# Kernel optimization log

Hardware: AMD Instinct MI355X
Metric: run time of the kernel (lower is better)

Reference implementation:

```python
import jax, jax.numpy as jnp
import numpy as np
from jax import lax

DIM = 96
D_STATE = 16
D_CONV = 4
EXPAND = 2
D_INNER = EXPAND * DIM           # 192
DT_RANK = (DIM + 15) // 16       # 6
EPS = 1e-5


def _upsample2x_align_corners(x):
    # bilinear, align_corners=True, scale_factor=2 (matches nn.Upsample)
    B, C, H, W = x.shape
    def lin_idx(n_in, n_out):
        pos = jnp.arange(n_out) * ((n_in - 1) / (n_out - 1))
        i0 = jnp.floor(pos).astype(jnp.int32)
        i1 = jnp.minimum(i0 + 1, n_in - 1)
        w = (pos - i0).astype(x.dtype)
        return i0, i1, w
    r0, r1, rw = lin_idx(H, 2 * H)
    c0, c1, cw = lin_idx(W, 2 * W)
    xr = x[:, :, r0, :] * (1 - rw)[None, None, :, None] + x[:, :, r1, :] * rw[None, None, :, None]
    return xr[:, :, :, c0] * (1 - cw) + xr[:, :, :, c1] * cw


def _conv2d(x, w, b, pad):
    y = lax.conv_general_dilated(x, w, (1, 1), [(pad, pad), (pad, pad)],
                                 dimension_numbers=('NCHW', 'OIHW', 'NCHW'))
    return y + b[None, :, None, None]


def _instance_norm(x):
    m = x.mean(axis=(2, 3), keepdims=True)
    v = x.var(axis=(2, 3), keepdims=True)
    return (x - m) * lax.rsqrt(v + EPS)


def _selective_scan(u, dt, A, Bm, Cm, D):
    # u, dt: [B,L,Din]; Bm, Cm: [B,L,N]; A: [Din,N]; D: [Din]
    def step(h, inp):
        u_t, dt_t, B_t, C_t = inp                       # [B,Din],[B,Din],[B,N],[B,N]
        dA = jnp.exp(dt_t[..., None] * A)               # [B,Din,N]
        h = h * dA + (dt_t * u_t)[..., None] * B_t[:, None, :]
        y = jnp.einsum('bdn,bn->bd', h, C_t)
        return h, y
    Bsz, L, Din = u.shape
    h0 = jnp.zeros((Bsz, Din, A.shape[1]), u.dtype)
    xs = (u.swapaxes(0, 1), dt.swapaxes(0, 1), Bm.swapaxes(0, 1), Cm.swapaxes(0, 1))
    _, ys = lax.scan(step, h0, xs)                      # ys: [L,B,Din]
    return ys.swapaxes(0, 1) + u * D


def _mamba(xseq, in_proj_w, conv1d_w, conv1d_b, x_proj_w, dt_proj_w, dt_proj_b,
           A_log, D, out_proj_w):
    # xseq: [B,L,dim]
    xz = xseq @ in_proj_w.T                             # [B,L,2*Din]
    xin, z = jnp.split(xz, 2, axis=-1)
    xc = xin.swapaxes(1, 2)                             # [B,Din,L]
    xc = lax.conv_general_dilated(xc, conv1d_w, (1,), [(D_CONV - 1, 0)],
                                  dimension_numbers=('NCH', 'OIH', 'NCH'),
                                  feature_group_count=D_INNER)
    xc = xc + conv1d_b[None, :, None]
    u = jax.nn.silu(xc.swapaxes(1, 2))                  # [B,L,Din]
    x_dbl = u @ x_proj_w.T                              # [B,L,dt_rank+2N]
    dt, Bm, Cm = jnp.split(x_dbl, [DT_RANK, DT_RANK + D_STATE], axis=-1)
    dt = jax.nn.softplus(dt @ dt_proj_w.T + dt_proj_b)  # [B,L,Din]
    A = -jnp.exp(A_log)                                 # [Din,N]
    y = _selective_scan(u, dt, A, Bm, Cm, D)
    y = y * jax.nn.silu(z)
    return y @ out_proj_w.T                             # [B,L,dim]


def setup_inputs() -> dict:
    key = jax.random.key(0)
    ks = jax.random.split(key, 16)
    s = 0.05
    inp = {
        'x': jax.random.normal(ks[0], (2, DIM, 64, 64), jnp.float32),
        'Hx': jax.random.normal(ks[1], (2, DIM * 2, 128, 128), jnp.float32),
        'conv1_w': jax.random.normal(ks[2], (DIM, DIM * 3, 1, 1), jnp.float32) * s,
        'conv1_b': jax.random.normal(ks[3], (DIM,), jnp.float32) * s,
        'conv2_w': jax.random.normal(ks[4], (DIM, DIM, 3, 3), jnp.float32) * s,
        'conv2_b': jax.random.normal(ks[5], (DIM,), jnp.float32) * s,
        'conv3_w': jax.random.normal(ks[6], (DIM, DIM, 1, 1), jnp.float32) * s,
        'conv3_b': jax.random.normal(ks[7], (DIM,), jnp.float32) * s,
        'in_proj_w': jax.random.normal(ks[8], (2 * D_INNER, DIM), jnp.float32) * s,
        'conv1d_w': jax.random.normal(ks[9], (D_INNER, 1, D_CONV), jnp.float32) * s,
        'conv1d_b': jax.random.normal(ks[10], (D_INNER,), jnp.float32) * s,
        'x_proj_w': jax.random.normal(ks[11], (DT_RANK + 2 * D_STATE, D_INNER), jnp.float32) * s,
        'dt_proj_w': jax.random.normal(ks[12], (D_INNER, DT_RANK), jnp.float32) * s,
        'dt_proj_b': jax.random.normal(ks[13], (D_INNER,), jnp.float32) * 0.1,
        'A_log': jnp.log(jnp.tile(jnp.arange(1, D_STATE + 1, dtype=jnp.float32)[None, :], (D_INNER, 1))),
        'D': jnp.ones((D_INNER,), jnp.float32),
        'out_proj_w': jax.random.normal(ks[14], (DIM, D_INNER), jnp.float32) * s,
    }
    return inp


def reference(x, Hx, conv1_w, conv1_b, conv2_w, conv2_b, conv3_w, conv3_b,
              in_proj_w, conv1d_w, conv1d_b, x_proj_w, dt_proj_w, dt_proj_b,
              A_log, D, out_proj_w):
    up = _upsample2x_align_corners(x)                   # [B,dim,H,W]
    cat = jnp.concatenate([up, Hx], axis=1)             # [B,3*dim,H,W]
    h = _conv2d(cat, conv1_w, conv1_b, 0)
    h = _conv2d(h, conv2_w, conv2_b, 1)
    h = _conv2d(h, conv3_w, conv3_b, 0)
    Lx = jax.nn.selu(_instance_norm(h))                 # [B,dim,H,W]
    B, C, H, W = Lx.shape
    seq = Lx.reshape(B, C, H * W).swapaxes(1, 2)        # [B,L,dim]
    y = _mamba(seq, in_proj_w, conv1d_w, conv1d_b, x_proj_w, dt_proj_w,
               dt_proj_b, A_log, D, out_proj_w)
    return y.swapaxes(1, 2).reshape(B, C, H, W) + Lx
```

## Files before the change

kernel.cpp:

```cpp
#include <hip/hip_runtime.h>
#include <hip/hip_bf16.h>
#include <math.h>

#define LSEQ 16384
#define DIN  192
#define GCH  512
#define TCH  32

typedef float f4v __attribute__((ext_vector_type(4)));
typedef short s8v __attribute__((ext_vector_type(8)));
typedef unsigned short u16x8 __attribute__((ext_vector_type(8)));

__device__ __forceinline__ float siluf(float x) { return x / (1.0f + __expf(-x)); }
__device__ __forceinline__ unsigned short f2bf(float f) {
  unsigned int u = __float_as_uint(f);
  unsigned int r = (u + 0x7FFFu + ((u >> 16) & 1u)) >> 16;
  return (unsigned short)r;
}
__device__ __forceinline__ float bf2f(unsigned short s) {
  return __uint_as_float(((unsigned int)s) << 16);
}

__global__ __launch_bounds__(256) void k_packw(const float* __restrict__ c1w,
    const float* __restrict__ c2w, const float* __restrict__ c3w,
    const float* __restrict__ Win, const float* __restrict__ Wx,
    const float* __restrict__ Wout, unsigned short* __restrict__ P) {
  int i = blockIdx.x * 256 + threadIdx.x;
  if (i >= 184320) return;
  if (i < 27648) { P[i] = f2bf(c1w[i]); return; }
  int j = i - 27648;
  if (j < 82944) {
    int cc = j / 27648, r = j - cc * 27648;
    int kk = r / 3072, r2 = r - kk * 3072;
    int oc = r2 >> 5, icl = r2 & 31;
    int ky = kk / 3, kx = kk - ky * 3;
    P[i] = f2bf(c2w[((oc * 96 + cc * 32 + icl) * 3 + ky) * 3 + kx]);
    return;
  }
  j -= 82944;
  if (j < 9216) { P[i] = f2bf(c3w[j]); return; }
  j -= 9216;
  if (j < 36864) { P[i] = f2bf(Win[j]); return; }
  j -= 36864;
  if (j < 9216) {
    int oc = j / 192, k = j - oc * 192;
    P[i] = (oc < 38) ? f2bf(Wx[oc * 192 + k]) : (unsigned short)0;
    return;
  }
  j -= 9216;
  P[i] = f2bf(Wout[j]);
}

__global__ __launch_bounds__(256) void k_upsample(const float* __restrict__ x, float* __restrict__ up) {
  int idx = blockIdx.x * 256 + threadIdx.x;
  if (idx >= 2 * 96 * LSEQ) return;
  int ow = idx & 127, oh = (idx >> 7) & 127, bc = idx >> 14;
  float pr = oh * (63.0f / 127.0f); int r0 = (int)pr; float rw = pr - (float)r0; int r1 = min(r0 + 1, 63);
  float pc = ow * (63.0f / 127.0f); int c0 = (int)pc; float cw = pc - (float)c0; int c1 = min(c0 + 1, 63);
  const float* xp = x + (size_t)bc * 4096;
  float v00 = xp[r0 * 64 + c0], v01 = xp[r0 * 64 + c1];
  float v10 = xp[r1 * 64 + c0], v11 = xp[r1 * 64 + c1];
  float top = v00 + (v10 - v00) * rw;
  float bot = v01 + (v11 - v01) * rw;
  up[idx] = top + (bot - top) * cw;
}

#define SRC_PLANAR2 0
#define SRC_ROWS    1
#define OUT_BF16R    0
#define OUT_F32P     1
#define OUT_F32R     2
#define OUT_F32P_RES 4
#define OUT_XZ       5

template<int SM, int OM, int NT>
__global__ __launch_bounds__(256) void k_gemm(
    const void* __restrict__ xa, const void* __restrict__ xb, int CA,
    const unsigned short* __restrict__ Wp, const float* __restrict__ bias,
    void* __restrict__ outv, void* __restrict__ outv2, const float* __restrict__ resid,
    int K, int ostride, int ng) {
  __shared__ unsigned short x_t[128 * 96];
  __shared__ unsigned short w_t[NT * 16 * 96];
  Wp += (size_t)blockIdx.y * 96 * K;
  int pxg0 = blockIdx.x * 128;
  int b = pxg0 >> 14, px_in0 = pxg0 & 16383;
  int tid = threadIdx.x, lane = tid & 63, wv = tid >> 6;
  int r = lane & 15, q = lane >> 4;
  f4v acc[2][NT];
#pragma unroll
  for (int mi = 0; mi < 2; mi++)
#pragma unroll
    for (int n = 0; n < NT; n++) acc[mi][n] = (f4v)0.0f;
  int nchunk = K / 96;
  for (int kc = 0; kc < nchunk; kc++) {
    for (int t = tid; t < NT * 16 * 12; t += 256) {
      int row = t / 12, u8 = t - row * 12;
      *(u16x8*)&w_t[row * 96 + u8 * 8] = *(const u16x8*)&Wp[(size_t)row * K + kc * 96 + u8 * 8];
    }
    if (SM == SRC_PLANAR2) {
      const float* A0 = (const float*)xa;
      const float* A1 = (const float*)xb;
      int CB = K - CA;
      for (int t = tid; t < 3072; t += 256) {
        int px4 = t / 96, c_l = t - px4 * 96;
        int c = kc * 96 + c_l;
        const float* sp = (c < CA) ? (A0 + ((size_t)b * CA + c) * LSEQ + px_in0 + px4 * 4)
                                   : (A1 + ((size_t)b * CB + (c - CA)) * LSEQ + px_in0 + px4 * 4);
        float4 v = *(const float4*)sp;
        x_t[(px4 * 4 + 0) * 96 + c_l] = f2bf(v.x);
        x_t[(px4 * 4 + 1) * 96 + c_l] = f2bf(v.y);
        x_t[(px4 * 4 + 2) * 96 + c_l] = f2bf(v.z);
        x_t[(px4 * 4 + 3) * 96 + c_l] = f2bf(v.w);
      }
    } else {
      const unsigned short* X = (const unsigned short*)xa;
      for (int t = tid; t < 1536; t += 256) {
        int rr = t / 12, u8 = t - rr * 12;
        *(u16x8*)&x_t[rr * 96 + u8 * 8] =
            *(const u16x8*)&X[(size_t)(pxg0 + rr) * K + kc * 96 + u8 * 8];
      }
    }
    __syncthreads();
#pragma unroll
    for (int k0 = 0; k0 < 96; k0 += 32) {
      s8v a0 = *(const s8v*)&x_t[((wv * 2 + 0) * 16 + r) * 96 + k0 + q * 8];
      s8v a1 = *(const s8v*)&x_t[((wv * 2 + 1) * 16 + r) * 96 + k0 + q * 8];
#pragma unroll
      for (int n = 0; n < NT; n++) {
        s8v bb = *(const s8v*)&w_t[(n * 16 + r) * 96 + k0 + q * 8];
        acc[0][n] = __builtin_amdgcn_mfma_f32_16x16x32_bf16(a0, bb, acc[0][n], 0, 0, 0);
        acc[1][n] = __builtin_amdgcn_mfma_f32_16x16x32_bf16(a1, bb, acc[1][n], 0, 0, 0);
      }
    }
    __syncthreads();
  }
#pragma unroll
  for (int mi = 0; mi < 2; mi++) {
    int pxl = (wv * 2 + mi) * 16 + q * 4;
    int pxg = pxg0 + pxl;
#pragma unroll
    for (int n = 0; n < NT; n++) {
      int oc = n * 16 + r;
      if (OM == OUT_BF16R) {
        float bv = bias[oc];
        unsigned short* O = (unsigned short*)outv;
#pragma unroll
        for (int g = 0; g < 4; g++)
          O[(size_t)(pxg + g) * 96 + oc] = f2bf(acc[mi][n][g] + bv);
      } else if (OM == OUT_F32P) {
        float bv = bias[oc];
        float* O = (float*)outv;
        float4 o = make_float4(acc[mi][n][0] + bv, acc[mi][n][1] + bv,
                               acc[mi][n][2] + bv, acc[mi][n][3] + bv);
        *(float4*)&O[((size_t)b * 96 + oc) * LSEQ + px_in0 + pxl] = o;
      } else if (OM == OUT_F32P_RES) {
        float* O = (float*)outv;
        size_t ad = ((size_t)b * 96 + oc) * LSEQ + px_in0 + pxl;
        float4 rv = *(const float4*)&resid[ad];
        float4 o = make_float4(acc[mi][n][0] + rv.x, acc[mi][n][1] + rv.y,
                               acc[mi][n][2] + rv.z, acc[mi][n][3] + rv.w);
        *(float4*)&O[ad] = o;
      } else if (OM == OUT_F32R) {
        float* O = (float*)outv;
        int ocg = blockIdx.y * 96 + oc;
        if (ocg < ng) {
#pragma unroll
          for (int g = 0; g < 4; g++)
            O[(size_t)(pxg + g) * ostride + ocg] = acc[mi][n][g];
        }
      } else {
        int ocg = (blockIdx.y & 1) * 96 + oc;
        if (blockIdx.y < 2) {
          float* O = (float*)outv;
#pragma unroll
          for (int g = 0; g < 4; g++)
            O[(size_t)(pxg + g) * 192 + ocg] = acc[mi][n][g];
        } else {
          unsigned short* O = (unsigned short*)outv2;
#pragma unroll
          for (int g = 0; g < 4; g++)
            O[(size_t)(pxg + g) * 192 + ocg] = f2bf(acc[mi][n][g]);
        }
      }
    }
  }
}

__global__ __launch_bounds__(256) void k_conv3x3m(const unsigned short* __restrict__ X,
    const unsigned short* __restrict__ Wp2, const float* __restrict__ bias,
    unsigned short* __restrict__ out) {
  __shared__ unsigned short in_t[3 * 68 * 32];
  __shared__ unsigned short w_t[9 * 96 * 32];
  int bi = blockIdx.x;
  int hx = bi & 1, y = (bi >> 1) & 127, b = bi >> 8;
  int px0 = hx * 64;
  int tid = threadIdx.x, lane = tid & 63, wv = tid >> 6;
  int r = lane & 15, q = lane >> 4;
  f4v acc[6];
#pragma unroll
  for (int n = 0; n < 6; n++) acc[n] = (f4v)0.0f;
  for (int cc = 0; cc < 3; cc++) {
    for (int t = tid; t < 3456; t += 256)
      *(u16x8*)&w_t[t * 8] = *(const u16x8*)&Wp2[cc * 27648 + t * 8];
    for (int t = tid; t < 792; t += 256) {
      int row = t / 264, rem = t - row * 264;
      int c_l = rem >> 2, icq = rem & 3;
      int gy = y - 1 + row, gx = px0 - 1 + c_l;
      u16x8 v = {0, 0, 0, 0, 0, 0, 0, 0};
      if (gy >= 0 && gy < 128 && gx >= 0 && gx < 128)
        v = *(const u16x8*)&X[(((size_t)b * 128 + gy) * 128 + gx) * 96 + cc * 32 + icq * 8];
      *(u16x8*)&in_t[(row * 68 + c_l) * 32 + icq * 8] = v;
    }
    __syncthreads();
#pragma unroll
    for (int kk = 0; kk < 9; kk++) {
      int ky = kk / 3, kx = kk - ky * 3;
      s8v a = *(const s8v*)&in_t[(ky * 68 + wv * 16 + r + kx) * 32 + q * 8];
#pragma unroll
      for (int n = 0; n < 6; n++) {
        s8v bb = *(const s8v*)&w_t[(kk * 96 + n * 16 + r) * 32 + q * 8];
        acc[n] = __builtin_amdgcn_mfma_f32_16x16x32_bf16(a, bb, acc[n], 0, 0, 0);
      }
    }
    __syncthreads();
  }
  size_t rowbase = ((size_t)b * 128 + y) * 128 + px0 + wv * 16 + q * 4;
#pragma unroll
  for (int n = 0; n < 6; n++) {
    int oc = n * 16 + r;
    float bv = bias[oc];
#pragma unroll
    for (int g = 0; g < 4; g++)
      out[(rowbase + g) * 96 + oc] = f2bf(acc[n][g] + bv);
  }
}

__global__ __launch_bounds__(256) void k_stats(const float* __restrict__ h, float* __restrict__ stats) {
  int bc = blockIdx.x;
  const float* p = h + (size_t)bc * LSEQ;
  float s = 0.f, ss = 0.f;
  for (int i = threadIdx.x; i < LSEQ; i += 256) { float v = p[i]; s += v; ss = fmaf(v, v, ss); }
  __shared__ float rs[256], rss[256];
  int tid = threadIdx.x;
  rs[tid] = s; rss[tid] = ss; __syncthreads();
  for (int o = 128; o > 0; o >>= 1) {
    if (tid < o) { rs[tid] += rs[tid + o]; rss[tid] += rss[tid + o]; }
    __syncthreads();
  }
  if (tid == 0) {
    float m = rs[0] * (1.0f / LSEQ);
    float var = rss[0] * (1.0f / LSEQ) - m * m;
    stats[bc * 2] = m;
    stats[bc * 2 + 1] = rsqrtf(fmaxf(var, 0.f) + 1e-5f);
  }
}

__global__ __launch_bounds__(256) void k_normselu2(const float* __restrict__ h,
    const float* __restrict__ stats, float* __restrict__ Lx, unsigned short* __restrict__ LxR) {
  __shared__ float tile[96 * 65];
  int px0 = blockIdx.x * 64, b = blockIdx.y;
  int tid = threadIdx.x;
  const float kS = 1.0507009873554805f, kA = 1.6732632423543772f;
  for (int t = tid; t < 1536; t += 256) {
    int c = t >> 4, p4 = t & 15;
    size_t ga = ((size_t)b * 96 + c) * LSEQ + px0 + p4 * 4;
    float4 v = *(const float4*)&h[ga];
    float m = stats[(b * 96 + c) * 2], rv = stats[(b * 96 + c) * 2 + 1];
    v.x = (v.x - m) * rv; v.y = (v.y - m) * rv; v.z = (v.z - m) * rv; v.w = (v.w - m) * rv;
    v.x = v.x > 0.f ? kS * v.x : kS * kA * expm1f(v.x);
    v.y = v.y > 0.f ? kS * v.y : kS * kA * expm1f(v.y);
    v.z = v.z > 0.f ? kS * v.z : kS * kA * expm1f(v.z);
    v.w = v.w > 0.f ? kS * v.w : kS * kA * expm1f(v.w);
    *(float4*)&Lx[ga] = v;
    tile[c * 65 + p4 * 4 + 0] = v.x;
    tile[c * 65 + p4 * 4 + 1] = v.y;
    tile[c * 65 + p4 * 4 + 2] = v.z;
    tile[c * 65 + p4 * 4 + 3] = v.w;
  }
  __syncthreads();
  for (int t = tid; t < 768; t += 256) {
    int px = t / 12, c8 = t - px * 12;
    u16x8 o;
#pragma unroll
    for (int jj = 0; jj < 8; jj++) o[jj] = f2bf(tile[(c8 * 8 + jj) * 65 + px]);
    *(u16x8*)&LxR[((size_t)b * LSEQ + px0 + px) * 96 + c8 * 8] = o;
  }
}

__global__ __launch_bounds__(256) void k_conv1d(const float* __restrict__ xzx,
    const float* __restrict__ w1d, const float* __restrict__ b1d,
    float* __restrict__ u, unsigned short* __restrict__ uR) {
  int gid = blockIdx.x * 256 + threadIdx.x;
  if (gid >= 2 * LSEQ * DIN) return;
  int d = gid % DIN, bl = gid / DIN;
  int l = bl & (LSEQ - 1);
  float4 w = *(const float4*)&w1d[d * 4];
  float wv[4] = {w.x, w.y, w.z, w.w};
  float acc = b1d[d];
#pragma unroll
  for (int k = 0; k < 4; k++) {
    int lk = l - 3 + k;
    if (lk >= 0) acc = fmaf(wv[k], xzx[(size_t)(bl - 3 + k) * DIN + d], acc);
  }
  float s = siluf(acc);
  u[gid] = s;
  uR[gid] = f2bf(s);
}

__global__ __launch_bounds__(192) void k_scanA(const float* __restrict__ u,
    const float* __restrict__ xdbl, const float* __restrict__ Wdt,
    const float* __restrict__ bdt, const float* __restrict__ Alog,
    float* __restrict__ chA, float* __restrict__ chB) {
  int b = blockIdx.y, g = blockIdx.x, d = threadIdx.x;
  __shared__ float Bs[TCH * 16], Dts[TCH * 8];
  for (int i = d; i < TCH * 16; i += 192) {
    int t = i >> 4, n = i & 15;
    Bs[i] = xdbl[(size_t)(b * LSEQ + g * TCH + t) * 38 + 6 + n];
  }
  for (int i = d; i < TCH * 6; i += 192) {
    int t = i / 6, c = i - t * 6;
    Dts[t * 8 + c] = xdbl[(size_t)(b * LSEQ + g * TCH + t) * 38 + c];
  }
  float ac[16];
#pragma unroll
  for (int n = 0; n < 16; n++) ac[n] = -__expf(Alog[d * 16 + n]);
  float wdt[6];
#pragma unroll
  for (int c = 0; c < 6; c++) wdt[c] = Wdt[d * 6 + c];
  float bd = bdt[d];
  __syncthreads();
  float ap[16], hb[16];
#pragma unroll
  for (int n = 0; n < 16; n++) { ap[n] = 1.f; hb[n] = 0.f; }
  for (int t = 0; t < TCH; t++) {
    size_t base = (size_t)(b * LSEQ + g * TCH + t);
    float uv = u[base * DIN + d];
    float dtraw = bd;
#pragma unroll
    for (int c = 0; c < 6; c++) dtraw = fmaf(Dts[t * 8 + c], wdt[c], dtraw);
    float dtv = dtraw > 20.f ? dtraw : log1pf(__expf(dtraw));
    float du = dtv * uv;
    float bs[16];
    const float4* src = (const float4*)&Bs[t * 16];
#pragma unroll
    for (int qq = 0; qq < 4; qq++) {
      float4 v = src[qq];
      bs[qq * 4] = v.x; bs[qq * 4 + 1] = v.y; bs[qq * 4 + 2] = v.z; bs[qq * 4 + 3] = v.w;
    }
#pragma unroll
    for (int n = 0; n < 16; n++) {
      float e = __expf(dtv * ac[n]);
      ap[n] *= e;
      hb[n] = fmaf(hb[n], e, du * bs[n]);
    }
  }
  size_t co = ((size_t)(b * GCH + g) * DIN + d) * 16;
#pragma unroll
  for (int qq = 0; qq < 4; qq++) {
    ((float4*)(chA + co))[qq] = make_float4(ap[qq * 4], ap[qq * 4 + 1], ap[qq * 4 + 2], ap[qq * 4 + 3]);
    ((float4*)(chB + co))[qq] = make_float4(hb[qq * 4], hb[qq * 4 + 1], hb[qq * 4 + 2], hb[qq * 4 + 3]);
  }
}

__global__ __launch_bounds__(256) void k_scanB(const float* __restrict__ chA,
    const float* __restrict__ chB, float* __restrict__ h0) {
  __shared__ float sa[16 * 17], sb[16 * 17];
  int blk = blockIdx.x;
  int b = blk / DIN, d = blk - b * DIN;
  int tid = threadIdx.x;
  int seg = tid >> 4, n = tid & 15;
  float ca[32], cb[32];
  float aagg = 1.f, bagg = 0.f;
#pragma unroll 8
  for (int j = 0; j < 32; j++) {
    int g = seg * 32 + j;
    size_t off = ((size_t)(b * GCH + g) * DIN + d) * 16 + n;
    float a = chA[off], bb = chB[off];
    ca[j] = a; cb[j] = bb;
    bagg = fmaf(a, bagg, bb);
    aagg *= a;
  }
  sa[n * 17 + seg] = aagg;
  sb[n * 17 + seg] = bagg;
  __syncthreads();
  if (tid < 16) {
    float pa = 1.f, pb = 0.f;
#pragma unroll
    for (int s = 0; s < 16; s++) {
      float ta = sa[tid * 17 + s], tb = sb[tid * 17 + s];
      sa[tid * 17 + s] = pa;
      sb[tid * 17 + s] = pb;
      pb = fmaf(ta, pb, tb);
      pa *= ta;
    }
  }
  __syncthreads();
  float h = sb[n * 17 + seg];
#pragma unroll 8
  for (int j = 0; j < 32; j++) {
    int g = seg * 32 + j;
    size_t off = ((size_t)(b * GCH + g) * DIN + d) * 16 + n;
    h0[off] = h;
    h = fmaf(ca[j], h, cb[j]);
  }
}

__global__ __launch_bounds__(192) void k_scanC(const float* __restrict__ u,
    const float* __restrict__ xdbl, const float* __restrict__ Wdt,
    const float* __restrict__ bdt, const unsigned short* __restrict__ zR,
    const float* __restrict__ Alog, const float* __restrict__ Dp,
    const float* __restrict__ h0, unsigned short* __restrict__ yR) {
  int b = blockIdx.y, g = blockIdx.x, d = threadIdx.x;
  __shared__ float Bs[TCH * 16], Cs[TCH * 16], Dts[TCH * 8];
  for (int i = d; i < TCH * 16; i += 192) {
    int t = i >> 4, n = i & 15;
    size_t rb = (size_t)(b * LSEQ + g * TCH + t) * 38;
    Bs[i] = xdbl[rb + 6 + n];
    Cs[i] = xdbl[rb + 22 + n];
  }
  for (int i = d; i < TCH * 6; i += 192) {
    int t = i / 6, c = i - t * 6;
    Dts[t * 8 + c] = xdbl[(size_t)(b * LSEQ + g * TCH + t) * 38 + c];
  }
  float ac[16];
#pragma unroll
  for (int n = 0; n < 16; n++) ac[n] = -__expf(Alog[d * 16 + n]);
  float wdt[6];
#pragma unroll
  for (int c = 0; c < 6; c++) wdt[c] = Wdt[d * 6 + c];
  float bd = bdt[d];
  float Dd = Dp[d];
  __syncthreads();
  size_t co = ((size_t)(b * GCH + g) * DIN + d) * 16;
  float h[16];
#pragma unroll
  for (int qq = 0; qq < 4; qq++) {
    float4 v = ((const float4*)(h0 + co))[qq];
    h[qq * 4] = v.x; h[qq * 4 + 1] = v.y; h[qq * 4 + 2] = v.z; h[qq * 4 + 3] = v.w;
  }
  for (int t = 0; t < TCH; t++) {
    size_t base = (size_t)(b * LSEQ + g * TCH + t);
    float uv = u[base * DIN + d];
    float zv = bf2f(zR[base * DIN + d]);
    float dtraw = bd;
#pragma unroll
    for (int c = 0; c < 6; c++) dtraw = fmaf(Dts[t * 8 + c], wdt[c], dtraw);
    float dtv = dtraw > 20.f ? dtraw : log1pf(__expf(dtraw));
    float du = dtv * uv;
    float bs[16], cs[16];
    const float4* sb = (const float4*)&Bs[t * 16];
    const float4* sc = (const float4*)&Cs[t * 16];
#pragma unroll
    for (int qq = 0; qq < 4; qq++) {
      float4 vb = sb[qq], vc = sc[qq];
      bs[qq * 4] = vb.x; bs[qq * 4 + 1] = vb.y; bs[qq * 4 + 2] = vb.z; bs[qq * 4 + 3] = vb.w;
      cs[qq * 4] = vc.x; cs[qq * 4 + 1] = vc.y; cs[qq * 4 + 2] = vc.z; cs[qq * 4 + 3] = vc.w;
    }
    float y0 = 0.f, y1 = 0.f, y2 = 0.f, y3 = 0.f;
#pragma unroll
    for (int n = 0; n < 16; n++) {
      float e = __expf(dtv * ac[n]);
      h[n] = fmaf(h[n], e, du * bs[n]);
      float p = h[n] * cs[n];
      if ((n & 3) == 0) y0 += p; else if ((n & 3) == 1) y1 += p;
      else if ((n & 3) == 2) y2 += p; else y3 += p;
    }
    float yv = ((y0 + y1) + (y2 + y3)) + uv * Dd;
    yR[base * DIN + d] = f2bf(yv * siluf(zv));
  }
}

extern "C" void kernel_launch(void* const* d_in, const int* in_sizes, int n_in,
                              void* d_out, int out_size, void* d_ws, size_t ws_size,
                              hipStream_t stream) {
  (void)in_sizes; (void)n_in; (void)out_size; (void)ws_size;
  const float* x    = (const float*)d_in[0];
  const float* Hx   = (const float*)d_in[1];
  const float* c1w  = (const float*)d_in[2];
  const float* c1b  = (const float*)d_in[3];
  const float* c2w  = (const float*)d_in[4];
  const float* c2b  = (const float*)d_in[5];
  const float* c3w  = (const float*)d_in[6];
  const float* c3b  = (const float*)d_in[7];
  const float* Win  = (const float*)d_in[8];
  const float* w1d  = (const float*)d_in[9];
  const float* b1d  = (const float*)d_in[10];
  const float* Wx   = (const float*)d_in[11];
  const float* Wdt  = (const float*)d_in[12];
  const float* bdt  = (const float*)d_in[13];
  const float* Alog = (const float*)d_in[14];
  const float* Dp   = (const float*)d_in[15];
  const float* Wout = (const float*)d_in[16];
  float* out = (float*)d_out;

  float* ws = (float*)d_ws;
  const size_t F = (size_t)2 * 96 * LSEQ;
  const size_t Fh = F / 2;

  float*          b_up = ws;
  float*          b_h3 = ws;
  float*          chA  = ws;
  float*          b_Lx = ws + F;
  unsigned short* R1   = (unsigned short*)(ws + 2 * F);
  unsigned short* R2   = (unsigned short*)(ws + 2 * F + Fh);
  float*          xdbl = ws + 2 * F + Fh;
  float*          xzx  = ws + 3 * F;
  float*          chB  = ws + 3 * F;
  float*          h0b  = ws + 4 * F;
  unsigned short* zRb  = (unsigned short*)(ws + 5 * F);
  unsigned short* R3   = (unsigned short*)(ws + 6 * F);
  float*          b_u  = ws + 7 * F;
  unsigned short* Wp   = (unsigned short*)(ws + 9 * F);
  float*          b_st = ws + 9 * F + 92160;

  k_packw<<<dim3(720), dim3(256), 0, stream>>>(c1w, c2w, c3w, Win, Wx, Wout, Wp);
  k_upsample<<<dim3(12288), dim3(256), 0, stream>>>(x, b_up);
  k_gemm<SRC_PLANAR2, OUT_BF16R, 6><<<dim3(256, 1), dim3(256), 0, stream>>>(
      b_up, Hx, 96, Wp, c1b, R1, nullptr, nullptr, 288, 0, 0);
  k_conv3x3m<<<dim3(512), dim3(256), 0, stream>>>(R1, Wp + 27648, c2b, R2);
  k_gemm<SRC_ROWS, OUT_F32P, 6><<<dim3(256, 1), dim3(256), 0, stream>>>(
      R2, nullptr, 0, Wp + 110592, c3b, b_h3, nullptr, nullptr, 96, 0, 0);
  k_stats<<<dim3(192), dim3(256), 0, stream>>>(b_h3, b_st);
  k_normselu2<<<dim3(256, 2), dim3(256), 0, stream>>>(b_h3, b_st, b_Lx, R1);
  k_gemm<SRC_ROWS, OUT_XZ, 6><<<dim3(256, 4), dim3(256), 0, stream>>>(
      R1, nullptr, 0, Wp + 119808, nullptr, xzx, zRb, nullptr, 96, 192, 0);
  k_conv1d<<<dim3((2 * LSEQ * DIN + 255) / 256), dim3(256), 0, stream>>>(xzx, w1d, b1d, b_u, R3);
  k_gemm<SRC_ROWS, OUT_F32R, 3><<<dim3(256, 1), dim3(256), 0, stream>>>(
      R3, nullptr, 0, Wp + 156672, nullptr, xdbl, nullptr, nullptr, 192, 38, 38);
  k_scanA<<<dim3(GCH, 2), dim3(192), 0, stream>>>(b_u, xdbl, Wdt, bdt, Alog, chA, chB);
  k_scanB<<<dim3(2 * DIN), dim3(256), 0, stream>>>(chA, chB, h0b);
  k_scanC<<<dim3(GCH, 2), dim3(192), 0, stream>>>(b_u, xdbl, Wdt, bdt, zRb, Alog, Dp, h0b, R3);
  k_gemm<SRC_ROWS, OUT_F32P_RES, 6><<<dim3(256, 1), dim3(256), 0, stream>>>(
      R3, nullptr, 0, Wp + 165888, nullptr, out, nullptr, b_Lx, 192, 0, 0);
}
```

Before: 380.6 us.

## Fuse upsample into conv1 GEMM load and streamline scan math

New measurement: 348.7 us. 8.4% less time.

```diff
diff --git a/kernel.cpp b/kernel.cpp
--- a/kernel.cpp
+++ b/kernel.cpp
@@ -11,7 +11,14 @@
 typedef short s8v __attribute__((ext_vector_type(8)));
 typedef unsigned short u16x8 __attribute__((ext_vector_type(8)));
 
-__device__ __forceinline__ float siluf(float x) { return x / (1.0f + __expf(-x)); }
+__device__ __forceinline__ float siluf(float x) { return __fdividef(x, 1.0f + __expf(-x)); }
+__device__ __forceinline__ float fexp2(float x) {
+#if __has_builtin(__builtin_amdgcn_exp2f)
+  return __builtin_amdgcn_exp2f(x);
+#else
+  return __expf(x * 0.69314718056f);
+#endif
+}
 __device__ __forceinline__ unsigned short f2bf(float f) {
   unsigned int u = __float_as_uint(f);
   unsigned int r = (u + 0x7FFFu + ((u >> 16) & 1u)) >> 16;
@@ -51,22 +58,9 @@
   P[i] = f2bf(Wout[j]);
 }
 
-__global__ __launch_bounds__(256) void k_upsample(const float* __restrict__ x, float* __restrict__ up) {
-  int idx = blockIdx.x * 256 + threadIdx.x;
-  if (idx >= 2 * 96 * LSEQ) return;
-  int ow = idx & 127, oh = (idx >> 7) & 127, bc = idx >> 14;
-  float pr = oh * (63.0f / 127.0f); int r0 = (int)pr; float rw = pr - (float)r0; int r1 = min(r0 + 1, 63);
-  float pc = ow * (63.0f / 127.0f); int c0 = (int)pc; float cw = pc - (float)c0; int c1 = min(c0 + 1, 63);
-  const float* xp = x + (size_t)bc * 4096;
-  float v00 = xp[r0 * 64 + c0], v01 = xp[r0 * 64 + c1];
-  float v10 = xp[r1 * 64 + c0], v11 = xp[r1 * 64 + c1];
-  float top = v00 + (v10 - v00) * rw;
-  float bot = v01 + (v11 - v01) * rw;
-  up[idx] = top + (bot - top) * cw;
-}
-
 #define SRC_PLANAR2 0
 #define SRC_ROWS    1
+#define SRC_UPCAT   2
 #define OUT_BF16R    0
 #define OUT_F32P     1
 #define OUT_F32R     2
@@ -111,6 +105,38 @@
         x_t[(px4 * 4 + 1) * 96 + c_l] = f2bf(v.y);
         x_t[(px4 * 4 + 2) * 96 + c_l] = f2bf(v.z);
         x_t[(px4 * 4 + 3) * 96 + c_l] = f2bf(v.w);
+      }
+    } else if (SM == SRC_UPCAT) {
+      const float* X0 = (const float*)xa;
+      const float* HX = (const float*)xb;
+      for (int t = tid; t < 3072; t += 256) {
+        int px4 = t / 96, c_l = t - px4 * 96;
+        int c = kc * 96 + c_l;
+        int pxl = px4 * 4;
+        if (c < 96) {
+          int pxg = px_in0 + pxl;
+          int oh = pxg >> 7, ow0 = pxg & 127;
+          float pr = oh * (63.0f / 127.0f);
+          int r0 = (int)pr; float rw = pr - (float)r0; int r1 = min(r0 + 1, 63);
+          const float* rp0 = X0 + ((size_t)b * 96 + c) * 4096 + r0 * 64;
+          const float* rp1 = X0 + ((size_t)b * 96 + c) * 4096 + r1 * 64;
+#pragma unroll
+          for (int g = 0; g < 4; g++) {
+            int ow = ow0 + g;
+            float pc = ow * (63.0f / 127.0f);
+            int c0 = (int)pc; float cw = pc - (float)c0; int c1 = min(c0 + 1, 63);
+            float v00 = rp0[c0], v01 = rp0[c1], v10 = rp1[c0], v11 = rp1[c1];
+            float top = v00 + (v10 - v00) * rw;
+            float bot = v01 + (v11 - v01) * rw;
+            x_t[(pxl + g) * 96 + c_l] = f2bf(top + (bot - top) * cw);
+          }
+        } else {
+          float4 v = *(const float4*)&HX[((size_t)b * 192 + (c - 96)) * LSEQ + px_in0 + pxl];
+          x_t[(pxl + 0) * 96 + c_l] = f2bf(v.x);
+          x_t[(pxl + 1) * 96 + c_l] = f2bf(v.y);
+          x_t[(pxl + 2) * 96 + c_l] = f2bf(v.z);
+          x_t[(pxl + 3) * 96 + c_l] = f2bf(v.w);
+        }
       }
     } else {
       const unsigned short* X = (const unsigned short*)xa;
@@ -255,22 +281,24 @@
   }
 }
 
+__device__ __forceinline__ float seluf(float v) {
+  const float kS = 1.0507009873554805f, kSA = 1.0507009873554805f * 1.6732632423543772f;
+  return v > 0.f ? kS * v : kSA * (__expf(v) - 1.f);
+}
 __global__ __launch_bounds__(256) void k_normselu2(const float* __restrict__ h,
     const float* __restrict__ stats, float* __restrict__ Lx, unsigned short* __restrict__ LxR) {
   __shared__ float tile[96 * 65];
   int px0 = blockIdx.x * 64, b = blockIdx.y;
   int tid = threadIdx.x;
-  const float kS = 1.0507009873554805f, kA = 1.6732632423543772f;
   for (int t = tid; t < 1536; t += 256) {
     int c = t >> 4, p4 = t & 15;
     size_t ga = ((size_t)b * 96 + c) * LSEQ + px0 + p4 * 4;
     float4 v = *(const float4*)&h[ga];
     float m = stats[(b * 96 + c) * 2], rv = stats[(b * 96 + c) * 2 + 1];
-    v.x = (v.x - m) * rv; v.y = (v.y - m) * rv; v.z = (v.z - m) * rv; v.w = (v.w - m) * rv;
-    v.x = v.x > 0.f ? kS * v.x : kS * kA * expm1f(v.x);
-    v.y = v.y > 0.f ? kS * v.y : kS * kA * expm1f(v.y);
-    v.z = v.z > 0.f ? kS * v.z : kS * kA * expm1f(v.z);
-    v.w = v.w > 0.f ? kS * v.w : kS * kA * expm1f(v.w);
+    v.x = seluf((v.x - m) * rv);
+    v.y = seluf((v.y - m) * rv);
+    v.z = seluf((v.z - m) * rv);
+    v.w = seluf((v.w - m) * rv);
     *(float4*)&Lx[ga] = v;
     tile[c * 65 + p4 * 4 + 0] = v.x;
     tile[c * 65 + p4 * 4 + 1] = v.y;
@@ -307,7 +335,7 @@
   uR[gid] = f2bf(s);
 }
 
-__global__ __launch_bounds__(192) void k_scanA(const float* __restrict__ u,
+__global__ __launch_bounds__(192, 3) void k_scanA(const float* __restrict__ u,
     const float* __restrict__ xdbl, const float* __restrict__ Wdt,
     const float* __restrict__ bdt, const float* __restrict__ Alog,
     float* __restrict__ chA, float* __restrict__ chB) {
@@ -321,25 +349,32 @@
     int t = i / 6, c = i - t * 6;
     Dts[t * 8 + c] = xdbl[(size_t)(b * LSEQ + g * TCH + t) * 38 + c];
   }
-  float ac[16];
-#pragma unroll
-  for (int n = 0; n < 16; n++) ac[n] = -__expf(Alog[d * 16 + n]);
+  float ac2[16];
+#pragma unroll
+  for (int n = 0; n < 16; n++) ac2[n] = -__expf(Alog[d * 16 + n]) * 1.44269504f;
   float wdt[6];
 #pragma unroll
   for (int c = 0; c < 6; c++) wdt[c] = Wdt[d * 6 + c];
   float bd = bdt[d];
+  size_t base0 = (size_t)(b * LSEQ + g * TCH);
+  float uu[TCH];
+#pragma unroll
+  for (int t = 0; t < TCH; t++) uu[t] = u[(base0 + t) * DIN + d];
   __syncthreads();
+  float dtv[TCH];
+#pragma unroll
+  for (int t = 0; t < TCH; t++) {
+    float dr = bd;
+#pragma unroll
+    for (int c = 0; c < 6; c++) dr = fmaf(Dts[t * 8 + c], wdt[c], dr);
+    dtv[t] = dr > 20.f ? dr : __logf(1.f + __expf(dr));
+  }
   float ap[16], hb[16];
 #pragma unroll
   for (int n = 0; n < 16; n++) { ap[n] = 1.f; hb[n] = 0.f; }
   for (int t = 0; t < TCH; t++) {
-    size_t base = (size_t)(b * LSEQ + g * TCH + t);
-    float uv = u[base * DIN + d];
-    float dtraw = bd;
-#pragma unroll
-    for (int c = 0; c < 6; c++) dtraw = fmaf(Dts[t * 8 + c], wdt[c], dtraw);
-    float dtv = dtraw > 20.f ? dtraw : log1pf(__expf(dtraw));
-    float du = dtv * uv;
+    float dl2 = dtv[t] * 1.f;
+    float du = dtv[t] * uu[t];
     float bs[16];
     const float4* src = (const float4*)&Bs[t * 16];
 #pragma unroll
@@ -349,7 +384,7 @@
     }
 #pragma unroll
     for (int n = 0; n < 16; n++) {
-      float e = __expf(dtv * ac[n]);
+      float e = fexp2(dl2 * ac2[n]);
       ap[n] *= e;
       hb[n] = fmaf(hb[n], e, du * bs[n]);
     }
@@ -405,7 +440,7 @@
   }
 }
 
-__global__ __launch_bounds__(192) void k_scanC(const float* __restrict__ u,
+__global__ __launch_bounds__(192, 3) void k_scanC(const float* __restrict__ u,
     const float* __restrict__ xdbl, const float* __restrict__ Wdt,
     const float* __restrict__ bdt, const unsigned short* __restrict__ zR,
     const float* __restrict__ Alog, const float* __restrict__ Dp,
@@ -422,15 +457,18 @@
     int t = i / 6, c = i - t * 6;
     Dts[t * 8 + c] = xdbl[(size_t)(b * LSEQ + g * TCH + t) * 38 + c];
   }
-  float ac[16];
-#pragma unroll
-  for (int n = 0; n < 16; n++) ac[n] = -__expf(Alog[d * 16 + n]);
+  float ac2[16];
+#pragma unroll
+  for (int n = 0; n < 16; n++) ac2[n] = -__expf(Alog[d * 16 + n]) * 1.44269504f;
   float wdt[6];
 #pragma unroll
   for (int c = 0; c < 6; c++) wdt[c] = Wdt[d * 6 + c];
   float bd = bdt[d];
   float Dd = Dp[d];
-  __syncthreads();
+  size_t base0 = (size_t)(b * LSEQ + g * TCH);
+  float uu[TCH];
+#pragma unroll
+  for (int t = 0; t < TCH; t++) uu[t] = u[(base0 + t) * DIN + d];
   size_t co = ((size_t)(b * GCH + g) * DIN + d) * 16;
   float h[16];
 #pragma unroll
@@ -438,35 +476,38 @@
     float4 v = ((const float4*)(h0 + co))[qq];
     h[qq * 4] = v.x; h[qq * 4 + 1] = v.y; h[qq * 4 + 2] = v.z; h[qq * 4 + 3] = v.w;
   }
+  __syncthreads();
+  float dtv[TCH];
+#pragma unroll
   for (int t = 0; t < TCH; t++) {
-    size_t base = (size_t)(b * LSEQ + g * TCH + t);
-    float uv = u[base * DIN + d];
-    float zv = bf2f(zR[base * DIN + d]);
-    float dtraw = bd;
-#pragma unroll
-    for (int c = 0; c < 6; c++) dtraw = fmaf(Dts[t * 8 + c], wdt[c], dtraw);
-    float dtv = dtraw > 20.f ? dtraw : log1pf(__expf(dtraw));
-    float du = dtv * uv;
+    float dr = bd;
+#pragma unroll
+    for (int c = 0; c < 6; c++) dr = fmaf(Dts[t * 8 + c], wdt[c], dr);
+    dtv[t] = dr > 20.f ? dr : __logf(1.f + __expf(dr));
+  }
+  for (int t = 0; t < TCH; t++) {
+    float du = dtv[t] * uu[t];
+    float zv = bf2f(zR[(base0 + t) * DIN + d]);
     float bs[16], cs[16];
-    const float4* sb = (const float4*)&Bs[t * 16];
-    const float4* sc = (const float4*)&Cs[t * 16];
+    const float4* sbp = (const float4*)&Bs[t * 16];
+    const float4* scp = (const float4*)&Cs[t * 16];
 #pragma unroll
     for (int qq = 0; qq < 4; qq++) {
-      float4 vb = sb[qq], vc = sc[qq];
+      float4 vb = sbp[qq], vc = scp[qq];
       bs[qq * 4] = vb.x; bs[qq * 4 + 1] = vb.y; bs[qq * 4 + 2] = vb.z; bs[qq * 4 + 3] = vb.w;
       cs[qq * 4] = vc.x; cs[qq * 4 + 1] = vc.y; cs[qq * 4 + 2] = vc.z; cs[qq * 4 + 3] = vc.w;
     }
     float y0 = 0.f, y1 = 0.f, y2 = 0.f, y3 = 0.f;
 #pragma unroll
     for (int n = 0; n < 16; n++) {
-      float e = __expf(dtv * ac[n]);
+      float e = fexp2(dtv[t] * ac2[n]);
       h[n] = fmaf(h[n], e, du * bs[n]);
       float p = h[n] * cs[n];
       if ((n & 3) == 0) y0 += p; else if ((n & 3) == 1) y1 += p;
       else if ((n & 3) == 2) y2 += p; else y3 += p;
     }
-    float yv = ((y0 + y1) + (y2 + y3)) + uv * Dd;
-    yR[base * DIN + d] = f2bf(yv * siluf(zv));
+    float yv = ((y0 + y1) + (y2 + y3)) + uu[t] * Dd;
+    yR[(base0 + t) * DIN + d] = f2bf(yv * siluf(zv));
   }
 }
 
@@ -497,7 +538,6 @@
   const size_t F = (size_t)2 * 96 * LSEQ;
   const size_t Fh = F / 2;
 
-  float*          b_up = ws;
   float*          b_h3 = ws;
   float*          chA  = ws;
   float*          b_Lx = ws + F;
@@ -514,9 +554,8 @@
   float*          b_st = ws + 9 * F + 92160;
 
   k_packw<<<dim3(720), dim3(256), 0, stream>>>(c1w, c2w, c3w, Win, Wx, Wout, Wp);
-  k_upsample<<<dim3(12288), dim3(256), 0, stream>>>(x, b_up);
-  k_gemm<SRC_PLANAR2, OUT_BF16R, 6><<<dim3(256, 1), dim3(256), 0, stream>>>(
-      b_up, Hx, 96, Wp, c1b, R1, nullptr, nullptr, 288, 0, 0);
+  k_gemm<SRC_UPCAT, OUT_BF16R, 6><<<dim3(256, 1), dim3(256), 0, stream>>>(
+      x, Hx, 96, Wp, c1b, R1, nullptr, nullptr, 288, 0, 0);
   k_conv3x3m<<<dim3(512), dim3(256), 0, stream>>>(R1, Wp + 27648, c2b, R2);
   k_gemm<SRC_ROWS, OUT_F32P, 6><<<dim3(256, 1), dim3(256), 0, stream>>>(
       R2, nullptr, 0, Wp + 110592, c3b, b_h3, nullptr, nullptr, 96, 0, 0);
```
